# Kernel optimization log

Hardware: AMD Instinct MI355X
Metric: run time of the kernel (lower is better)

## Reference

```python
import jax, jax.numpy as jnp
import numpy as np

N_HEADS = 8
N_LANDMARKS = 64
NEWTON_ITERS = 6


def _iterative_inv(mat):
    # mat: [B,H,L,L]; Newton-Schulz approximate inverse, 6 iterations
    L = mat.shape[-1]
    fro = jnp.sqrt(jnp.sum(mat * mat, axis=(-2, -1), keepdims=True))
    fro = jnp.maximum(fro, 1e-6)
    z = jnp.swapaxes(mat, -2, -1) / (fro * fro)
    for _ in range(NEWTON_ITERS):
        z = 2.0 * z - z @ mat @ z
    return z


def setup_inputs() -> dict:
    key = jax.random.key(0)
    ks = jax.random.split(key, 5)
    B, N, C = 4, 8192, 512
    s = 1.0 / np.sqrt(C)
    return {
        "x": jax.random.normal(ks[0], (B, N, C), jnp.float32),
        "Wqkv": jax.random.normal(ks[1], (3 * C, C), jnp.float32) * s,
        "bqkv": jax.random.normal(ks[2], (3 * C,), jnp.float32) * 0.01,
        "Wproj": jax.random.normal(ks[3], (C, C), jnp.float32) * s,
        "bproj": jax.random.normal(ks[4], (C,), jnp.float32) * 0.01,
    }


def reference(x, Wqkv, bqkv, Wproj, bproj):
    B, N, C = x.shape
    H = N_HEADS
    hd = C // H
    scale = hd ** (-0.5)
    n_lm = N_LANDMARKS

    qkv = x @ Wqkv.T + bqkv                       # [B,N,3C]
    qkv = qkv.reshape(B, N, 3, H, hd).transpose(2, 0, 3, 1, 4)  # [3,B,H,N,hd]
    q, k, v = qkv[0], qkv[1], qkv[2]

    if N <= n_lm:
        attn = jax.nn.softmax(q @ jnp.swapaxes(k, -2, -1) * scale, axis=-1)
        out = attn @ v
    else:
        stride = max(N // n_lm, 1)
        lm_idx = jnp.arange(0, N, stride)[:n_lm]
        q_lm = q[:, :, lm_idx]                    # [B,H,L,hd]
        k_lm = k[:, :, lm_idx]
        kernel_1 = jax.nn.softmax(q @ jnp.swapaxes(k_lm, -2, -1) * scale, axis=-1)   # [B,H,N,L]
        kernel_2 = jax.nn.softmax(q_lm @ jnp.swapaxes(k_lm, -2, -1) * scale, axis=-1)  # [B,H,L,L]
        kernel_3 = jax.nn.softmax(q_lm @ jnp.swapaxes(k, -2, -1) * scale, axis=-1)   # [B,H,L,N]
        kernel_2_inv = _iterative_inv(kernel_2)
        out = kernel_1 @ (kernel_2_inv @ (kernel_3 @ v))  # [B,H,N,hd]

    out = jnp.swapaxes(out, 1, 2).reshape(B, N, C)
    return out @ Wproj.T + bproj
```

## Files before the change

kernel.cpp:

```cpp
#include <hip/hip_runtime.h>

typedef unsigned short u16;
typedef unsigned int u32;

typedef __bf16 v8bf __attribute__((ext_vector_type(8)));
typedef float v4f __attribute__((ext_vector_type(4)));
typedef u16 v8u __attribute__((ext_vector_type(8)));

#define N_TOK 8192
#define CDIM 512
#define HEADS 8
#define HD 64
#define LM 64
#define LSTRIDE 128
#define BHN 32
#define NCHUNK 16
#define SCALE 0.125f

__device__ __forceinline__ float b2f(u16 u) { return __uint_as_float(((u32)u) << 16); }
__device__ __forceinline__ u16 f2bf(float f) {
  u32 u = __float_as_uint(f);
  u += 0x7fffu + ((u >> 16) & 1u);
  return (u16)(u >> 16);
}
__device__ __forceinline__ u32 pk2bf(float a, float b) {
  return (u32)f2bf(a) | ((u32)f2bf(b) << 16);
}

__device__ __forceinline__ void gl_lds16(const u16* g, u16* l) {
  __builtin_amdgcn_global_load_lds(
      (const __attribute__((address_space(1))) u32*)g,
      (__attribute__((address_space(3))) u32*)l, 16, 0, 0);
}

__device__ __forceinline__ void wr_hl(u16* __restrict__ h, u16* __restrict__ l,
                                      int row, int col, float v) {
  u16 hi = f2bf(v);
  u16 lo = f2bf(v - b2f(hi));
  int a = row * 64 + (((col >> 3) ^ (row & 7)) << 3) + (col & 7);
  h[a] = hi;
  l[a] = lo;
}

__global__ __launch_bounds__(256) void cast_bf16(const float* __restrict__ src,
                                                 u16* __restrict__ dst, int n8) {
  int i = blockIdx.x * 256 + threadIdx.x;
  if (i >= n8) return;
  const float4* s = (const float4*)src;
  float4 a = s[(size_t)i * 2], b = s[(size_t)i * 2 + 1];
  uint4 o;
  o.x = (u32)f2bf(a.x) | ((u32)f2bf(a.y) << 16);
  o.y = (u32)f2bf(a.z) | ((u32)f2bf(a.w) << 16);
  o.z = (u32)f2bf(b.x) | ((u32)f2bf(b.y) << 16);
  o.w = (u32)f2bf(b.z) | ((u32)f2bf(b.w) << 16);
  *(uint4*)(dst + (size_t)i * 8) = o;
}

__global__ __launch_bounds__(256) void cast_w2(const float* __restrict__ wa,
                                               const float* __restrict__ wb,
                                               u16* __restrict__ da,
                                               u16* __restrict__ db) {
  int i = blockIdx.x * 256 + threadIdx.x;
  const float* src;
  u16* dst;
  int j;
  if (i < 98304) { src = wa; dst = da; j = i; }
  else           { src = wb; dst = db; j = i - 98304; }
  const float4* s = (const float4*)src;
  float4 a = s[(size_t)j * 2], b = s[(size_t)j * 2 + 1];
  uint4 o;
  o.x = (u32)f2bf(a.x) | ((u32)f2bf(a.y) << 16);
  o.y = (u32)f2bf(a.z) | ((u32)f2bf(a.w) << 16);
  o.z = (u32)f2bf(b.x) | ((u32)f2bf(b.y) << 16);
  o.w = (u32)f2bf(b.z) | ((u32)f2bf(b.w) << 16);
  *(uint4*)(dst + (size_t)j * 8) = o;
}

template <int MODE>
__global__ __launch_bounds__(256) void gemm_bt(const u16* __restrict__ A,
                                               const u16* __restrict__ Bm,
                                               const float* __restrict__ bias,
                                               u16* __restrict__ qo,
                                               u16* __restrict__ ko,
                                               u16* __restrict__ vo,
                                               float* __restrict__ outp) {
  __shared__ __align__(16) u16 As[128 * 32];
  __shared__ __align__(16) u16 Bs[128 * 32];
  const int K = 512;
  const int m0 = blockIdx.x * 128;
  const int n0 = blockIdx.y * 128;
  const int t = threadIdx.x;
  const int lane = t & 63, w = t >> 6;
  const int wm = w >> 1, wn = w & 1;
  const int quad = lane >> 4, lrow = lane & 15;

  v4f acc[4][4];
#pragma unroll
  for (int i = 0; i < 4; ++i)
#pragma unroll
    for (int j = 0; j < 4; ++j)
#pragma unroll
      for (int r = 0; r < 4; ++r) acc[i][j][r] = 0.f;

  for (int kt = 0; kt < K; kt += 32) {
    __syncthreads();
#pragma unroll
    for (int p = 0; p < 2; ++p) {
      int ci = p * 256 + t;
      int r = ci >> 2, s = ci & 3;
      int cs = (s ^ (r >> 1)) & 3;
      gl_lds16(A + (size_t)(m0 + r) * K + kt + cs * 8, &As[ci * 8]);
      gl_lds16(Bm + (size_t)(n0 + r) * K + kt + cs * 8, &Bs[ci * 8]);
    }
    __syncthreads();
    v8bf af[4], bf[4];
#pragma unroll
    for (int ti = 0; ti < 4; ++ti) {
      int row = wm * 64 + ti * 16 + lrow;
      af[ti] = *(const v8bf*)&As[row * 32 + ((quad ^ (row >> 1)) & 3) * 8];
    }
#pragma unroll
    for (int tj = 0; tj < 4; ++tj) {
      int row = wn * 64 + tj * 16 + lrow;
      bf[tj] = *(const v8bf*)&Bs[row * 32 + ((quad ^ (row >> 1)) & 3) * 8];
    }
#pragma unroll
    for (int ti = 0; ti < 4; ++ti)
#pragma unroll
      for (int tj = 0; tj < 4; ++tj)
        acc[ti][tj] = __builtin_amdgcn_mfma_f32_16x16x32_bf16(af[ti], bf[tj], acc[ti][tj], 0, 0, 0);
  }

#pragma unroll
  for (int ti = 0; ti < 4; ++ti) {
#pragma unroll
    for (int tj = 0; tj < 4; ++tj) {
      int gn = n0 + wn * 64 + tj * 16 + lrow;
      float bv = bias[gn];
#pragma unroll
      for (int r = 0; r < 4; ++r) {
        int gm = m0 + wm * 64 + ti * 16 + quad * 4 + r;
        float val = acc[ti][tj][r] + bv;
        if (MODE == 0) {
          int tt = gn >> 9;
          int h = (gn >> 6) & 7;
          int d = gn & 63;
          int b = gm >> 13;
          int n = gm & 8191;
          size_t di = ((size_t)(b * HEADS + h) * N_TOK + n) * HD + d;
          u16* dst = (tt == 0) ? qo : (tt == 1) ? ko : vo;
          dst[di] = f2bf(val);
        } else {
          outp[(size_t)gm * CDIM + gn] = val;
        }
      }
    }
  }
}

__global__ __launch_bounds__(256) void fpart(const u16* __restrict__ qb,
                                             const u16* __restrict__ kb,
                                             const u16* __restrict__ vb,
                                             float* __restrict__ Fp,
                                             float* __restrict__ Mc,
                                             float* __restrict__ Sc) {
  __shared__ __align__(16) char smem[4 * 64 * 40 * 2 * 2];
  __shared__ float msh[4][64], ssh[4][64];
  const int jc = blockIdx.x, bh = blockIdx.y;
  const int t = threadIdx.x;
  const int lane = t & 63, w = t >> 6;
  const int col = lane & 15, quad = lane >> 4;
  const int jq = lane & 7, dh = lane >> 3;

  u16* Pw = (u16*)smem + w * (64 * 40);
  u16* vT = (u16*)smem + 4 * (64 * 40) + w * (64 * 40);
  float* Fbuf = (float*)smem;

  v8bf qf[4][2];
#pragma unroll
  for (int it = 0; it < 4; ++it)
#pragma unroll
    for (int kh = 0; kh < 2; ++kh)
      qf[it][kh] = *(const v8bf*)(qb + ((size_t)bh * N_TOK + (size_t)(it * 16 + col) * LSTRIDE) * HD + kh * 32 + quad * 8);

  float mw[4], sw[4];
  v4f facc[4][4];
#pragma unroll
  for (int it = 0; it < 4; ++it) { mw[it] = -3.0e38f; sw[it] = 0.f; }
#pragma unroll
  for (int dt = 0; dt < 4; ++dt)
#pragma unroll
    for (int it = 0; it < 4; ++it)
#pragma unroll
      for (int r = 0; r < 4; ++r) facc[dt][it][r] = 0.f;

  const size_t kv0 = (size_t)bh * N_TOK + jc * 512 + w * 128;

  v8bf kf[2][2];
  v8u vr[4];
#pragma unroll
  for (int jt = 0; jt < 2; ++jt)
#pragma unroll
    for (int kh = 0; kh < 2; ++kh)
      kf[jt][kh] = *(const v8bf*)(kb + (kv0 + jt * 16 + col) * HD + kh * 32 + quad * 8);
#pragma unroll
  for (int e = 0; e < 4; ++e)
    vr[e] = *(const v8u*)(vb + (kv0 + jq * 4 + e) * HD + dh * 8);

#pragma unroll
  for (int st = 0; st < 4; ++st) {
#pragma unroll
    for (int e = 0; e < 8; ++e) {
      uint2 pk;
      pk.x = (u32)vr[0][e] | ((u32)vr[1][e] << 16);
      pk.y = (u32)vr[2][e] | ((u32)vr[3][e] << 16);
      *(uint2*)&vT[(dh * 8 + e) * 40 + jq * 4] = pk;
    }

    v8bf kfn[2][2];
    v8u vrn[4];
    if (st < 3) {
      const size_t bn = kv0 + (st + 1) * 32;
#pragma unroll
      for (int jt = 0; jt < 2; ++jt)
#pragma unroll
        for (int kh = 0; kh < 2; ++kh)
          kfn[jt][kh] = *(const v8bf*)(kb + (bn + jt * 16 + col) * HD + kh * 32 + quad * 8);
    }

    v4f sacc[2][4];
#pragma unroll
    for (int jt = 0; jt < 2; ++jt)
#pragma unroll
      for (int it = 0; it < 4; ++it) {
#pragma unroll
        for (int r = 0; r < 4; ++r) sacc[jt][it][r] = 0.f;
#pragma unroll
        for (int kh = 0; kh < 2; ++kh)
          sacc[jt][it] = __builtin_amdgcn_mfma_f32_16x16x32_bf16(kf[jt][kh], qf[it][kh], sacc[jt][it], 0, 0, 0);
      }

    if (st < 3) {
      const size_t bn = kv0 + (st + 1) * 32;
#pragma unroll
      for (int e = 0; e < 4; ++e)
        vrn[e] = *(const v8u*)(vb + (bn + jq * 4 + e) * HD + dh * 8);
    }

#pragma unroll
    for (int it = 0; it < 4; ++it) {
      float mloc = -3.0e38f;
#pragma unroll
      for (int jt = 0; jt < 2; ++jt)
#pragma unroll
        for (int r = 0; r < 4; ++r) {
          float s = sacc[jt][it][r] * SCALE;
          sacc[jt][it][r] = s;
          mloc = fmaxf(mloc, s);
        }
      mloc = fmaxf(mloc, __shfl_xor(mloc, 16));
      mloc = fmaxf(mloc, __shfl_xor(mloc, 32));
      float mnew = fmaxf(mw[it], mloc);
      float alpha = __expf(mw[it] - mnew);
      mw[it] = mnew;
      float rs = 0.f;
#pragma unroll
      for (int jt = 0; jt < 2; ++jt)
#pragma unroll
        for (int r = 0; r < 4; ++r) {
          float p = __expf(sacc[jt][it][r] - mnew);
          sacc[jt][it][r] = p;
          rs += p;
        }
      rs += __shfl_xor(rs, 16);
      rs += __shfl_xor(rs, 32);
      sw[it] = sw[it] * alpha + rs;
#pragma unroll
      for (int jt = 0; jt < 2; ++jt) {
        uint2 pk;
        pk.x = pk2bf(sacc[jt][it][0], sacc[jt][it][1]);
        pk.y = pk2bf(sacc[jt][it][2], sacc[jt][it][3]);
        *(uint2*)&Pw[(it * 16 + col) * 40 + jt * 16 + quad * 4] = pk;
      }
#pragma unroll
      for (int dt = 0; dt < 4; ++dt)
#pragma unroll
        for (int r = 0; r < 4; ++r) facc[dt][it][r] *= alpha;
    }

    v8bf vfr[4], pfr[4];
#pragma unroll
    for (int dt = 0; dt < 4; ++dt)
      vfr[dt] = *(const v8bf*)&vT[(dt * 16 + col) * 40 + quad * 8];
#pragma unroll
    for (int it = 0; it < 4; ++it)
      pfr[it] = *(const v8bf*)&Pw[(it * 16 + col) * 40 + quad * 8];
#pragma unroll
    for (int dt = 0; dt < 4; ++dt)
#pragma unroll
      for (int it = 0; it < 4; ++it)
        facc[dt][it] = __builtin_amdgcn_mfma_f32_16x16x32_bf16(vfr[dt], pfr[it], facc[dt][it], 0, 0, 0);

    if (st < 3) {
#pragma unroll
      for (int jt = 0; jt < 2; ++jt)
#pragma unroll
        for (int kh = 0; kh < 2; ++kh)
          kf[jt][kh] = kfn[jt][kh];
#pragma unroll
      for (int e = 0; e < 4; ++e) vr[e] = vrn[e];
    }
  }

  if (quad == 0) {
#pragma unroll
    for (int it = 0; it < 4; ++it) {
      msh[w][it * 16 + col] = mw[it];
      ssh[w][it * 16 + col] = sw[it];
    }
  }
  __syncthreads();

  const size_t cb = (size_t)(bh * NCHUNK + jc) * 64;
  float scl[4];
#pragma unroll
  for (int it = 0; it < 4; ++it) {
    int i = it * 16 + col;
    float m0 = msh[0][i], m1 = msh[1][i], m2 = msh[2][i], m3 = msh[3][i];
    float M = fmaxf(fmaxf(m0, m1), fmaxf(m2, m3));
    float e0 = __expf(m0 - M), e1 = __expf(m1 - M);
    float e2 = __expf(m2 - M), e3 = __expf(m3 - M);
    float Stot = e0 * ssh[0][i] + e1 * ssh[1][i] + e2 * ssh[2][i] + e3 * ssh[3][i];
    scl[it] = (w == 0) ? e0 : (w == 1) ? e1 : (w == 2) ? e2 : e3;
    if (w == 0 && quad == 0) {
      Mc[cb + i] = M;
      Sc[cb + i] = Stot;
    }
  }

  for (int wv = 0; wv < 4; ++wv) {
    if (w == wv) {
#pragma unroll
      for (int it = 0; it < 4; ++it)
#pragma unroll
        for (int dt = 0; dt < 4; ++dt) {
          float* dst = &Fbuf[(it * 16 + col) * 76 + dt * 16 + quad * 4];
          float4 v;
          v.x = facc[dt][it][0] * scl[it];
          v.y = facc[dt][it][1] * scl[it];
          v.z = facc[dt][it][2] * scl[it];
          v.w = facc[dt][it][3] * scl[it];
          if (wv == 0) {
            *(float4*)dst = v;
          } else {
            float4 o = *(float4*)dst;
            o.x += v.x; o.y += v.y; o.z += v.z; o.w += v.w;
            *(float4*)dst = o;
          }
        }
    }
    __syncthreads();
  }

  size_t base = (size_t)(bh * NCHUNK + jc) * 4096;
#pragma unroll
  for (int p = 0; p < 16; ++p) {
    int idx = p * 256 + t;
    Fp[base + idx] = Fbuf[(idx >> 6) * 76 + (idx & 63)];
  }
}

__device__ __forceinline__ void mm_hl(const u16* __restrict__ Ah,
                                      const u16* __restrict__ Al,
                                      const u16* __restrict__ Bh,
                                      const u16* __restrict__ Bl,
                                      int Ra, int quad, int lrow, v4f out[4]) {
  v8bf ah[2], al[2];
#pragma unroll
  for (int kk = 0; kk < 2; ++kk) {
    int c8 = (((kk * 4 + quad) ^ (Ra & 7)) * 8);
    ah[kk] = *(const v8bf*)&Ah[Ra * 64 + c8];
    al[kk] = *(const v8bf*)&Al[Ra * 64 + c8];
  }
#pragma unroll
  for (int nt = 0; nt < 4; ++nt) {
    int Rb = nt * 16 + lrow;
#pragma unroll
    for (int kk = 0; kk < 2; ++kk) {
      int c8 = (((kk * 4 + quad) ^ (Rb & 7)) * 8);
      v8bf bh = *(const v8bf*)&Bh[Rb * 64 + c8];
      v8bf bl = *(const v8bf*)&Bl[Rb * 64 + c8];
      out[nt] = __builtin_amdgcn_mfma_f32_16x16x32_bf16(ah[kk], bh, out[nt], 0, 0, 0);
      out[nt] = __builtin_amdgcn_mfma_f32_16x16x32_bf16(ah[kk], bl, out[nt], 0, 0, 0);
      out[nt] = __builtin_amdgcn_mfma_f32_16x16x32_bf16(al[kk], bh, out[nt], 0, 0, 0);
    }
  }
}

__global__ __launch_bounds__(256) void newton_t(const u16* __restrict__ qb,
                                                const u16* __restrict__ kb,
                                                const float* __restrict__ Fp,
                                                const float* __restrict__ Mc,
                                                const float* __restrict__ Sc,
                                                u16* __restrict__ Tt) {
  __shared__ float Sf[4096];
  __shared__ float red[4];
  __shared__ __align__(16) u16 mTh[4096], mTl[4096];
  __shared__ __align__(16) u16 zh_[4096], zl_[4096];
  __shared__ __align__(16) u16 zTh[4096], zTl[4096];
  __shared__ __align__(16) u16 wh_[4096], wl_[4096];
  const int bh = blockIdx.x;
  const int t = threadIdx.x, lane = t & 63, w = t >> 6;
  const int quad = lane >> 4, lrow = lane & 15;
  const int Ra = w * 16 + lrow;
  const int Rd = w * 16 + quad * 4;

  {
    v8bf qf[2], kf[4][2];
#pragma unroll
    for (int kk = 0; kk < 2; ++kk)
      qf[kk] = *(const v8bf*)(qb + ((size_t)bh * N_TOK + (size_t)Ra * LSTRIDE) * HD + kk * 32 + quad * 8);
#pragma unroll
    for (int nt = 0; nt < 4; ++nt)
#pragma unroll
      for (int kk = 0; kk < 2; ++kk)
        kf[nt][kk] = *(const v8bf*)(kb + ((size_t)bh * N_TOK + (size_t)(nt * 16 + lrow) * LSTRIDE) * HD + kk * 32 + quad * 8);
    v4f sa[4];
#pragma unroll
    for (int nt = 0; nt < 4; ++nt) {
#pragma unroll
      for (int r = 0; r < 4; ++r) sa[nt][r] = 0.f;
#pragma unroll
      for (int kk = 0; kk < 2; ++kk)
        sa[nt] = __builtin_amdgcn_mfma_f32_16x16x32_bf16(qf[kk], kf[nt][kk], sa[nt], 0, 0, 0);
    }
#pragma unroll
    for (int nt = 0; nt < 4; ++nt)
#pragma unroll
      for (int r = 0; r < 4; ++r)
        Sf[(Rd + r) * 64 + nt * 16 + lrow] = sa[nt][r] * SCALE;
  }
  __syncthreads();

  for (int rr = 0; rr < 16; ++rr) {
    int i = w * 16 + rr;
    float vv = Sf[i * 64 + lane];
    float m = vv;
#pragma unroll
    for (int off = 32; off; off >>= 1) m = fmaxf(m, __shfl_xor(m, off));
    float e = expf(vv - m);
    float s = e;
#pragma unroll
    for (int off = 32; off; off >>= 1) s += __shfl_xor(s, off);
    Sf[i * 64 + lane] = e / s;
  }
  __syncthreads();

  float loc = 0.f;
#pragma unroll
  for (int p = 0; p < 16; ++p) {
    float v = Sf[p * 256 + t];
    loc += v * v;
  }
#pragma unroll
  for (int off = 32; off; off >>= 1) loc += __shfl_xor(loc, off);
  if (lane == 0) red[w] = loc;
  __syncthreads();
  float fro = fmaxf(sqrtf(red[0] + red[1] + red[2] + red[3]), 1e-6f);
  float inv = 1.0f / (fro * fro);

  for (int p = 0; p < 16; ++p) {
    int idx = p * 256 + t;
    int r = idx >> 6, c = idx & 63;
    float Mrc = Sf[r * 64 + c];
    float Mcr = Sf[c * 64 + r];
    wr_hl(mTh, mTl, r, c, Mcr);
    wr_hl(zh_, zl_, r, c, Mcr * inv);
    wr_hl(zTh, zTl, r, c, Mrc * inv);
  }
  float zr[4][4];
#pragma unroll
  for (int nt = 0; nt < 4; ++nt)
#pragma unroll
    for (int r = 0; r < 4; ++r)
      zr[nt][r] = Sf[(nt * 16 + lrow) * 64 + Rd + r] * inv;
  __syncthreads();

  for (int it = 0; it < 6; ++it) {
    v4f aw[4];
#pragma unroll
    for (int nt = 0; nt < 4; ++nt)
#pragma unroll
      for (int r = 0; r < 4; ++r) aw[nt][r] = 0.f;
    mm_hl(zh_, zl_, mTh, mTl, Ra, quad, lrow, aw);
#pragma unroll
    for (int nt = 0; nt < 4; ++nt)
#pragma unroll
      for (int r = 0; r < 4; ++r)
        wr_hl(wh_, wl_, Rd + r, nt * 16 + lrow, aw[nt][r]);
    __syncthreads();

    v4f ap[4];
#pragma unroll
    for (int nt = 0; nt < 4; ++nt)
#pragma unroll
      for (int r = 0; r < 4; ++r) ap[nt][r] = 0.f;
    mm_hl(wh_, wl_, zTh, zTl, Ra, quad, lrow, ap);
    float znr[4][4];
#pragma unroll
    for (int nt = 0; nt < 4; ++nt)
#pragma unroll
      for (int r = 0; r < 4; ++r)
        znr[nt][r] = 2.f * zr[nt][r] - ap[nt][r];
    __syncthreads();

#pragma unroll
    for (int nt = 0; nt < 4; ++nt)
#pragma unroll
      for (int r = 0; r < 4; ++r) {
        zr[nt][r] = znr[nt][r];
        wr_hl(zh_, zl_, Rd + r, nt * 16 + lrow, znr[nt][r]);
        wr_hl(zTh, zTl, nt * 16 + lrow, Rd + r, znr[nt][r]);
      }
    __syncthreads();
  }

  if (t < 64) {
    float M = -3.0e38f;
#pragma unroll
    for (int jc = 0; jc < NCHUNK; ++jc)
      M = fmaxf(M, Mc[(bh * NCHUNK + jc) * 64 + t]);
    float S = 0.f;
#pragma unroll
    for (int jc = 0; jc < NCHUNK; ++jc)
      S += expf(Mc[(bh * NCHUNK + jc) * 64 + t] - M) * Sc[(bh * NCHUNK + jc) * 64 + t];
    float invS = 1.0f / S;
#pragma unroll
    for (int jc = 0; jc < NCHUNK; ++jc)
      Sf[jc * 64 + t] = expf(Mc[(bh * NCHUNK + jc) * 64 + t] - M) * invS;
  }
  __syncthreads();

  for (int p = 0; p < 16; ++p) {
    int idx = p * 256 + t;
    int i = idx >> 6, d = idx & 63;
    float sum = 0.f;
#pragma unroll
    for (int jc = 0; jc < NCHUNK; ++jc)
      sum += Sf[jc * 64 + i] * Fp[(size_t)(bh * NCHUNK + jc) * 4096 + idx];
    wr_hl(wh_, wl_, d, i, sum);
  }
  __syncthreads();

  v4f at[4];
#pragma unroll
  for (int nt = 0; nt < 4; ++nt)
#pragma unroll
    for (int r = 0; r < 4; ++r) at[nt][r] = 0.f;
  mm_hl(zh_, zl_, wh_, wl_, Ra, quad, lrow, at);
#pragma unroll
  for (int nt = 0; nt < 4; ++nt)
#pragma unroll
    for (int r = 0; r < 4; ++r)
      Tt[(size_t)bh * 4096 + (size_t)(nt * 16 + lrow) * 64 + (Rd + r)] = f2bf(at[nt][r]);
}

__global__ __launch_bounds__(256) void attn_out_k(const u16* __restrict__ qb,
                                                  const u16* __restrict__ kb,
                                                  const u16* __restrict__ Tt,
                                                  u16* __restrict__ ao) {
  __shared__ __align__(16) u16 Pl[4][1024];
  const int bh = blockIdx.y;
  const int b = bh >> 3, h = bh & 7;
  const int t = threadIdx.x;
  const int lane = t & 63, w = t >> 6;
  const int col = lane & 15, quad = lane >> 4;
  const int rot = (col & 7) * 8;

  v8bf kfr[4][2], tfr[4][2];
#pragma unroll
  for (int tj = 0; tj < 4; ++tj)
#pragma unroll
    for (int kh = 0; kh < 2; ++kh)
      kfr[tj][kh] = *(const v8bf*)(kb + ((size_t)bh * N_TOK + (size_t)(tj * 16 + col) * LSTRIDE) * HD + kh * 32 + quad * 8);
#pragma unroll
  for (int td = 0; td < 4; ++td)
#pragma unroll
    for (int jh = 0; jh < 2; ++jh)
      tfr[td][jh] = *(const v8bf*)(Tt + (size_t)bh * 4096 + (size_t)(td * 16 + col) * 64 + jh * 32 + quad * 8);

  u16* Pw = &Pl[w][0];

  for (int tile = 0; tile < 4; ++tile) {
    const int n0 = blockIdx.x * 256 + w * 64 + tile * 16;
    v8bf qf[2];
#pragma unroll
    for (int kh = 0; kh < 2; ++kh)
      qf[kh] = *(const v8bf*)(qb + ((size_t)bh * N_TOK + n0 + col) * HD + kh * 32 + quad * 8);

    v4f S[4];
#pragma unroll
    for (int tj = 0; tj < 4; ++tj) {
#pragma unroll
      for (int r = 0; r < 4; ++r) S[tj][r] = 0.f;
#pragma unroll
      for (int kh = 0; kh < 2; ++kh)
        S[tj] = __builtin_amdgcn_mfma_f32_16x16x32_bf16(kfr[tj][kh], qf[kh], S[tj], 0, 0, 0);
    }

    float mx = -3.0e38f;
#pragma unroll
    for (int tj = 0; tj < 4; ++tj)
#pragma unroll
      for (int r = 0; r < 4; ++r) {
        S[tj][r] *= SCALE;
        mx = fmaxf(mx, S[tj][r]);
      }
    mx = fmaxf(mx, __shfl_xor(mx, 16));
    mx = fmaxf(mx, __shfl_xor(mx, 32));
    float sum = 0.f;
#pragma unroll
    for (int tj = 0; tj < 4; ++tj)
#pragma unroll
      for (int r = 0; r < 4; ++r) {
        S[tj][r] = __expf(S[tj][r] - mx);
        sum += S[tj][r];
      }
    sum += __shfl_xor(sum, 16);
    sum += __shfl_xor(sum, 32);
    float inv = 1.0f / sum;

#pragma unroll
    for (int tj = 0; tj < 4; ++tj) {
      u32 lo = (u32)f2bf(S[tj][0] * inv) | ((u32)f2bf(S[tj][1] * inv) << 16);
      u32 hi = (u32)f2bf(S[tj][2] * inv) | ((u32)f2bf(S[tj][3] * inv) << 16);
      uint2 pk = {lo, hi};
      *(uint2*)&Pw[col * 64 + ((tj * 16 + quad * 4 + rot) & 63)] = pk;
    }
    v8bf pf[2];
#pragma unroll
    for (int jh = 0; jh < 2; ++jh)
      pf[jh] = *(const v8bf*)&Pw[col * 64 + ((jh * 32 + quad * 8 + rot) & 63)];

    v4f O[4];
#pragma unroll
    for (int td = 0; td < 4; ++td) {
#pragma unroll
      for (int r = 0; r < 4; ++r) O[td][r] = 0.f;
#pragma unroll
      for (int jh = 0; jh < 2; ++jh)
        O[td] = __builtin_amdgcn_mfma_f32_16x16x32_bf16(pf[jh], tfr[td][jh], O[td], 0, 0, 0);
    }
#pragma unroll
    for (int td = 0; td < 4; ++td)
#pragma unroll
      for (int r = 0; r < 4; ++r) {
        int n = n0 + quad * 4 + r;
        ao[((size_t)(b * N_TOK + n)) * CDIM + h * HD + td * 16 + col] = f2bf(O[td][r]);
      }
  }
}

__global__ void ws_too_small_sentinel(float* out) {
  if (threadIdx.x == 0 && blockIdx.x == 0) out[0] = 1.0f;
}

static constexpr size_t SZ_QKV = (size_t)BHN * N_TOK * HD * 2;
static constexpr size_t OFF_Q = 0;
static constexpr size_t OFF_K = OFF_Q + SZ_QKV;
static constexpr size_t OFF_V = OFF_K + SZ_QKV;
static constexpr size_t OFF_FP = OFF_V + SZ_QKV;
static constexpr size_t SZ_FP = (size_t)BHN * NCHUNK * 4096 * 4;
static constexpr size_t OFF_MC = OFF_FP + SZ_FP;
static constexpr size_t SZ_MS = (size_t)BHN * NCHUNK * 64 * 4;
static constexpr size_t OFF_SC = OFF_MC + SZ_MS;
static constexpr size_t OFF_T = OFF_SC + SZ_MS;
static constexpr size_t OFF_WQ = OFF_T + (size_t)BHN * 4096 * 2;
static constexpr size_t OFF_WP = OFF_WQ + (size_t)3 * CDIM * CDIM * 2;
static constexpr size_t OFF_END = OFF_WP + (size_t)CDIM * CDIM * 2;

extern "C" void kernel_launch(void* const* d_in, const int* in_sizes, int n_in,
                              void* d_out, int out_size, void* d_ws, size_t ws_size,
                              hipStream_t stream) {
  const float* x = (const float*)d_in[0];
  const float* Wqkv = (const float*)d_in[1];
  const float* bqkv = (const float*)d_in[2];
  const float* Wproj = (const float*)d_in[3];
  const float* bproj = (const float*)d_in[4];
  float* out = (float*)d_out;
  char* ws = (char*)d_ws;
  if (ws_size < OFF_END) {
    ws_too_small_sentinel<<<1, 64, 0, stream>>>(out);
    return;
  }

  u16* qb = (u16*)(ws + OFF_Q);
  u16* kb = (u16*)(ws + OFF_K);
  u16* vb = (u16*)(ws + OFF_V);
  float* Fp = (float*)(ws + OFF_FP);
  float* Mc = (float*)(ws + OFF_MC);
  float* Sc = (float*)(ws + OFF_SC);
  u16* Tt = (u16*)(ws + OFF_T);
  u16* Wqb = (u16*)(ws + OFF_WQ);
  u16* Wpb = (u16*)(ws + OFF_WP);
  u16* attn = (u16*)(ws + OFF_V);
  u16* xb = (u16*)d_out;

  cast_bf16<<<8192, 256, 0, stream>>>(x, xb, 2097152);
  cast_w2<<<512, 256, 0, stream>>>(Wqkv, Wproj, Wqb, Wpb);
  gemm_bt<0><<<dim3(256, 12), 256, 0, stream>>>(xb, Wqb, bqkv, qb, kb, vb, nullptr);
  fpart<<<dim3(NCHUNK, BHN), 256, 0, stream>>>(qb, kb, vb, Fp, Mc, Sc);
  newton_t<<<dim3(BHN), 256, 0, stream>>>(qb, kb, Fp, Mc, Sc, Tt);
  attn_out_k<<<dim3(32, BHN), 256, 0, stream>>>(qb, kb, Tt, attn);
  gemm_bt<1><<<dim3(256, 4), 256, 0, stream>>>(attn, Wpb, bproj, nullptr, nullptr, nullptr, out);
}
```

Before: 302.8 us.

## Fuse attention output with output projection GEMM via shared-memory tile

Merges the attention-output kernel and the projection GEMM into one kernel. Each block computes all 8 heads for 64 tokens into a swizzled 64x512 bf16 LDS tile, then multiplies it by Wproj, reading B fragments straight from global memory. This removes the bf16 attention round trip through HBM and one launch. In exchange the grid shrinks to 512 blocks, the LDS footprint grows to 64KB+, occupancy drops, and each block re-reads K landmarks, T and Wproj without LDS staging.

```diff
diff --git a/kernel.cpp b/kernel.cpp
--- a/kernel.cpp
+++ b/kernel.cpp
@@ -76,14 +76,12 @@
   *(uint4*)(dst + (size_t)j * 8) = o;
 }
 
-template <int MODE>
-__global__ __launch_bounds__(256) void gemm_bt(const u16* __restrict__ A,
-                                               const u16* __restrict__ Bm,
-                                               const float* __restrict__ bias,
-                                               u16* __restrict__ qo,
-                                               u16* __restrict__ ko,
-                                               u16* __restrict__ vo,
-                                               float* __restrict__ outp) {
+__global__ __launch_bounds__(256) void gemm_qkv(const u16* __restrict__ A,
+                                                const u16* __restrict__ Bm,
+                                                const float* __restrict__ bias,
+                                                u16* __restrict__ qo,
+                                                u16* __restrict__ ko,
+                                                u16* __restrict__ vo) {
   __shared__ __align__(16) u16 As[128 * 32];
   __shared__ __align__(16) u16 Bs[128 * 32];
   const int K = 512;
@@ -141,18 +139,14 @@
       for (int r = 0; r < 4; ++r) {
         int gm = m0 + wm * 64 + ti * 16 + quad * 4 + r;
         float val = acc[ti][tj][r] + bv;
-        if (MODE == 0) {
-          int tt = gn >> 9;
-          int h = (gn >> 6) & 7;
-          int d = gn & 63;
-          int b = gm >> 13;
-          int n = gm & 8191;
-          size_t di = ((size_t)(b * HEADS + h) * N_TOK + n) * HD + d;
-          u16* dst = (tt == 0) ? qo : (tt == 1) ? ko : vo;
-          dst[di] = f2bf(val);
-        } else {
-          outp[(size_t)gm * CDIM + gn] = val;
-        }
+        int tt = gn >> 9;
+        int h = (gn >> 6) & 7;
+        int d = gn & 63;
+        int b = gm >> 13;
+        int n = gm & 8191;
+        size_t di = ((size_t)(b * HEADS + h) * N_TOK + n) * HD + d;
+        u16* dst = (tt == 0) ? qo : (tt == 1) ? ko : vo;
+        dst[di] = f2bf(val);
       }
     }
   }
@@ -565,38 +559,40 @@
       Tt[(size_t)bh * 4096 + (size_t)(nt * 16 + lrow) * 64 + (Rd + r)] = f2bf(at[nt][r]);
 }
 
-__global__ __launch_bounds__(256) void attn_out_k(const u16* __restrict__ qb,
-                                                  const u16* __restrict__ kb,
-                                                  const u16* __restrict__ Tt,
-                                                  u16* __restrict__ ao) {
+__global__ __launch_bounds__(256) void attn_proj(const u16* __restrict__ qb,
+                                                 const u16* __restrict__ kb,
+                                                 const u16* __restrict__ Tt,
+                                                 const u16* __restrict__ Wpb,
+                                                 const float* __restrict__ bproj,
+                                                 float* __restrict__ outp) {
+  __shared__ __align__(16) u16 At[64 * 512];
   __shared__ __align__(16) u16 Pl[4][1024];
-  const int bh = blockIdx.y;
-  const int b = bh >> 3, h = bh & 7;
+  const int gid = blockIdx.x;
+  const int gm0 = gid * 64;
+  const int b = gm0 >> 13;
+  const int n0 = gm0 & 8191;
   const int t = threadIdx.x;
   const int lane = t & 63, w = t >> 6;
   const int col = lane & 15, quad = lane >> 4;
   const int rot = (col & 7) * 8;
-
-  v8bf kfr[4][2], tfr[4][2];
-#pragma unroll
-  for (int tj = 0; tj < 4; ++tj)
+  u16* Pw = &Pl[w][0];
+
+  for (int h = 0; h < HEADS; ++h) {
+    const int bh = b * HEADS + h;
+    v8bf kfr[4][2], tfr[4][2], qf[2];
+#pragma unroll
+    for (int tj = 0; tj < 4; ++tj)
+#pragma unroll
+      for (int kh = 0; kh < 2; ++kh)
+        kfr[tj][kh] = *(const v8bf*)(kb + ((size_t)bh * N_TOK + (size_t)(tj * 16 + col) * LSTRIDE) * HD + kh * 32 + quad * 8);
+#pragma unroll
+    for (int td = 0; td < 4; ++td)
+#pragma unroll
+      for (int jh = 0; jh < 2; ++jh)
+        tfr[td][jh] = *(const v8bf*)(Tt + (size_t)bh * 4096 + (size_t)(td * 16 + col) * 64 + jh * 32 + quad * 8);
 #pragma unroll
     for (int kh = 0; kh < 2; ++kh)
-      kfr[tj][kh] = *(const v8bf*)(kb + ((size_t)bh * N_TOK + (size_t)(tj * 16 + col) * LSTRIDE) * HD + kh * 32 + quad * 8);
-#pragma unroll
-  for (int td = 0; td < 4; ++td)
-#pragma unroll
-    for (int jh = 0; jh < 2; ++jh)
-      tfr[td][jh] = *(const v8bf*)(Tt + (size_t)bh * 4096 + (size_t)(td * 16 + col) * 64 + jh * 32 + quad * 8);
-
-  u16* Pw = &Pl[w][0];
-
-  for (int tile = 0; tile < 4; ++tile) {
-    const int n0 = blockIdx.x * 256 + w * 64 + tile * 16;
-    v8bf qf[2];
-#pragma unroll
-    for (int kh = 0; kh < 2; ++kh)
-      qf[kh] = *(const v8bf*)(qb + ((size_t)bh * N_TOK + n0 + col) * HD + kh * 32 + quad * 8);
+      qf[kh] = *(const v8bf*)(qb + ((size_t)bh * N_TOK + n0 + w * 16 + col) * HD + kh * 32 + quad * 8);
 
     v4f S[4];
 #pragma unroll
@@ -652,13 +648,55 @@
         O[td] = __builtin_amdgcn_mfma_f32_16x16x32_bf16(pf[jh], tfr[td][jh], O[td], 0, 0, 0);
     }
 #pragma unroll
-    for (int td = 0; td < 4; ++td)
+    for (int td = 0; td < 4; ++td) {
+      int colC = h * 64 + td * 16 + col;
 #pragma unroll
       for (int r = 0; r < 4; ++r) {
-        int n = n0 + quad * 4 + r;
-        ao[((size_t)(b * N_TOK + n)) * CDIM + h * HD + td * 16 + col] = f2bf(O[td][r]);
+        int tok = w * 16 + quad * 4 + r;
+        At[tok * 512 + (((colC >> 3) ^ (tok & 7)) << 3) + (colC & 7)] = f2bf(O[td][r]);
       }
-  }
+    }
+  }
+  __syncthreads();
+
+  v4f acc[4][8];
+#pragma unroll
+  for (int mf = 0; mf < 4; ++mf)
+#pragma unroll
+    for (int nf = 0; nf < 8; ++nf)
+#pragma unroll
+      for (int r = 0; r < 4; ++r) acc[mf][nf][r] = 0.f;
+
+  for (int kt = 0; kt < 512; kt += 32) {
+    v8bf af[4], bf[8];
+#pragma unroll
+    for (int mf = 0; mf < 4; ++mf) {
+      int row = mf * 16 + col;
+      int chunk = (kt >> 3) + quad;
+      af[mf] = *(const v8bf*)&At[row * 512 + ((chunk ^ (row & 7)) << 3)];
+    }
+#pragma unroll
+    for (int nf = 0; nf < 8; ++nf)
+      bf[nf] = *(const v8bf*)(Wpb + (size_t)(w * 128 + nf * 16 + col) * 512 + kt + quad * 8);
+#pragma unroll
+    for (int mf = 0; mf < 4; ++mf)
+#pragma unroll
+      for (int nf = 0; nf < 8; ++nf)
+        acc[mf][nf] = __builtin_amdgcn_mfma_f32_16x16x32_bf16(af[mf], bf[nf], acc[mf][nf], 0, 0, 0);
+  }
+
+#pragma unroll
+  for (int mf = 0; mf < 4; ++mf)
+#pragma unroll
+    for (int nf = 0; nf < 8; ++nf) {
+      int gn = w * 128 + nf * 16 + col;
+      float bv = bproj[gn];
+#pragma unroll
+      for (int r = 0; r < 4; ++r) {
+        int gm = gm0 + mf * 16 + quad * 4 + r;
+        outp[(size_t)gm * CDIM + gn] = acc[mf][nf][r] + bv;
+      }
+    }
 }
 
 __global__ void ws_too_small_sentinel(float* out) {
@@ -703,14 +741,12 @@
   u16* Tt = (u16*)(ws + OFF_T);
   u16* Wqb = (u16*)(ws + OFF_WQ);
   u16* Wpb = (u16*)(ws + OFF_WP);
-  u16* attn = (u16*)(ws + OFF_V);
   u16* xb = (u16*)d_out;
 
   cast_bf16<<<8192, 256, 0, stream>>>(x, xb, 2097152);
   cast_w2<<<512, 256, 0, stream>>>(Wqkv, Wproj, Wqb, Wpb);
-  gemm_bt<0><<<dim3(256, 12), 256, 0, stream>>>(xb, Wqb, bqkv, qb, kb, vb, nullptr);
+  gemm_qkv<<<dim3(256, 12), 256, 0, stream>>>(xb, Wqb, bqkv, qb, kb, vb);
   fpart<<<dim3(NCHUNK, BHN), 256, 0, stream>>>(qb, kb, vb, Fp, Mc, Sc);
   newton_t<<<dim3(BHN), 256, 0, stream>>>(qb, kb, Fp, Mc, Sc, Tt);
-  attn_out_k<<<dim3(32, BHN), 256, 0, stream>>>(qb, kb, Tt, attn);
-  gemm_bt<1><<<dim3(256, 4), 256, 0, stream>>>(attn, Wpb, bproj, nullptr, nullptr, nullptr, out);
-}
+  attn_proj<<<512, 256, 0, stream>>>(qb, kb, Tt, Wpb, bproj, out);
+}
```

Result: slower. 328.2 us (+8.4%).
